# Kernel optimization log

Measured on AMD Instinct MI355X. Metric: run time of the kernel, lower is better.

## Reference

```python
import jax, jax.numpy as jnp
import numpy as np

B, T, N_DYN, D_H, D_Z, HID = 256, 1024, 20, 64, 128, 64


def setup_inputs() -> dict:
    key = jax.random.key(0)
    ks = jax.random.split(key, 12)

    def uinit(k, shape):
        lim = 1.0 / np.sqrt(shape[0])
        return jax.random.uniform(k, shape, jnp.float32, -lim, lim)

    return dict(
        z0=jax.random.normal(ks[0], (B, D_Z), jnp.float32),
        # non-decreasing event times per sample (hours)
        t_dyn=jnp.cumsum(jax.random.uniform(ks[1], (B, T), jnp.float32), axis=1),
        Y_dyn=jax.random.normal(ks[2], (B, T, N_DYN), jnp.float32),
        M_dyn=jax.random.uniform(ks[3], (B, T, N_DYN), jnp.float32),
        H_dyn=jax.random.normal(ks[4], (B, T, D_H), jnp.float32),  # h_path.query(t_k) per step
        dyn_lens=jax.random.randint(ks[5], (B,), 0, T),
        ode_W0=uinit(ks[6], (D_Z, HID)), ode_b0=jnp.zeros((HID,), jnp.float32),
        ode_W1=uinit(ks[7], (HID, HID)), ode_b1=jnp.zeros((HID,), jnp.float32),
        ode_W2=uinit(ks[8], (HID, D_Z)), ode_b2=jnp.zeros((D_Z,), jnp.float32),
        W_ih=uinit(ks[9], (2 * N_DYN + D_H, 3 * D_Z)), b_ih=jnp.zeros((3 * D_Z,), jnp.float32),
        W_hh=uinit(ks[10], (D_Z, 3 * D_Z)), b_hh=jnp.zeros((3 * D_Z,), jnp.float32),
    )


def reference(z0, t_dyn, Y_dyn, M_dyn, H_dyn, dyn_lens,
              ode_W0, ode_b0, ode_W1, ode_b1, ode_W2, ode_b2,
              W_ih, b_ih, W_hh, b_hh):
    def ode_f(z):
        h = jnp.tanh(z @ ode_W0 + ode_b0)
        h = jnp.tanh(h @ ode_W1 + ode_b1)
        return h @ ode_W2 + ode_b2

    def evolve(z, dt):  # dt: (B,1); single-step RK4 of dz/ds = f(z)*dt over s in [0,1]
        f = lambda z_: ode_f(z_) * dt
        k1 = f(z)
        k2 = f(z + 0.5 * k1)
        k3 = f(z + 0.5 * k2)
        k4 = f(z + k3)
        return z + (k1 + 2.0 * k2 + 2.0 * k3 + k4) / 6.0

    def gru(x, h):  # torch GRUCell math
        gi = x @ W_ih + b_ih
        gh = h @ W_hh + b_hh
        i_r, i_u, i_n = jnp.split(gi, 3, axis=-1)
        h_r, h_u, h_n = jnp.split(gh, 3, axis=-1)
        r = jax.nn.sigmoid(i_r + h_r)
        u = jax.nn.sigmoid(i_u + h_u)
        n = jnp.tanh(i_n + r * h_n)
        return (1.0 - u) * n + u * h

    def step(carry, xs):
        z, t_prev = carry
        t_k, y_k, m_k, h_k, k = xs
        dt = jnp.clip(t_k - t_prev, 0.0)[:, None]
        # at k==0 dt is exactly 0 so evolve(z,0)==z, matching the torch k==0 branch
        z_ode = evolve(z, dt)
        inp = jnp.concatenate([y_k, m_k, h_k], axis=-1)  # (B, 2*n_dyn + d_h)
        z_new = gru(inp, z_ode)
        active = (k < dyn_lens).astype(z.dtype)[:, None]
        z = z_new * active + z_ode * (1.0 - active)
        return (z, t_k), z

    Tm = t_dyn.shape[1]
    xs = (t_dyn.T,
          jnp.transpose(Y_dyn, (1, 0, 2)),
          jnp.transpose(M_dyn, (1, 0, 2)),
          jnp.transpose(H_dyn, (1, 0, 2)),
          jnp.arange(Tm))
    (z_final, _), Z = jax.lax.scan(step, (z0, t_dyn[:, 0]), xs)
    return z_final, jnp.transpose(Z, (1, 0, 2))  # (B,d_z), (B,T,d_z)
```

## Files before the change

kernel.cpp:

```cpp
#include <hip/hip_runtime.h>
#include <cstdint>
#include <cstddef>

#define B_    256
#define T_    1024
#define NDYN  20
#define DH    64
#define DZ    128
#define HIDN  64
#define GCOLS 384
#define XDIM  104
#define THR   512

#define WHH_LDS_G 17
#define WHH_REGA  32
#define WHH_REGB  28

__device__ __forceinline__ int cpad(int k) { return (k >> 4) * 20 + (k & 15); }

#define BAR() do { asm volatile("s_waitcnt lgkmcnt(0)" ::: "memory"); \
                   __builtin_amdgcn_s_barrier(); } while (0)

template<int CTRL, int XORMASK>
__device__ __forceinline__ float dpp_sum(float v) {
#if __has_builtin(__builtin_amdgcn_mov_dpp)
  int o = __builtin_amdgcn_mov_dpp(__float_as_int(v), CTRL, 0xF, 0xF, true);
  return v + __int_as_float(o);
#else
  return v + __shfl_xor(v, XORMASK);
#endif
}

__device__ __forceinline__ float tanh_fast(float x) {
  float a = __expf(-2.f * fabsf(x));
  return copysignf((1.f - a) / (1.f + a), x);
}
__device__ __forceinline__ float sigm(float x) { return 1.f / (1.f + __expf(-x)); }

__global__ __launch_bounds__(THR, 1) void odernn_kernel(
    const float* __restrict__ z0, const float* __restrict__ tdyn,
    const float* __restrict__ Y, const float* __restrict__ Mm,
    const float* __restrict__ Hh, const int* __restrict__ lens,
    const float* __restrict__ W0, const float* __restrict__ b0,
    const float* __restrict__ W1, const float* __restrict__ b1,
    const float* __restrict__ W2, const float* __restrict__ b2,
    const float* __restrict__ Wih, const float* __restrict__ bih,
    const float* __restrict__ Whh, const float* __restrict__ bhh,
    const float* __restrict__ gi_pre, float* __restrict__ out, int use_gi)
{
  const int tid = threadIdx.x;
  const int b   = blockIdx.x;

  __shared__ __align__(16) float vinP[160];
  __shared__ __align__(16) float h1P[80];
  __shared__ __align__(16) float h2P[80];
  __shared__ __align__(16) float zodeL[128];
  __shared__ float zcurL[128];
  __shared__ float gateL[384];
  __shared__ float gateN[128];
  __shared__ float xsL[112];
  __shared__ float dtL[T_];
  __shared__ __align__(16) float4 WhhP4[WHH_LDS_G * 384];

  const int jg0 = tid >> 3, p0 = tid & 7;
  const int j2  = tid >> 2, p2 = tid & 3;
  const int gcol = (tid < GCOLS) ? tid : 0;

  float w0r[16], w1r[8], w2r[16], whhA[WHH_REGA], whhB[WHH_REGB];

  if (tid < GCOLS) {
    #pragma unroll 1
    for (int g = 0; g < WHH_LDS_G; ++g) {
      float4 w;
      w.x = Whh[(4 * g + 0) * GCOLS + tid];
      w.y = Whh[(4 * g + 1) * GCOLS + tid];
      w.z = Whh[(4 * g + 2) * GCOLS + tid];
      w.w = Whh[(4 * g + 3) * GCOLS + tid];
      WhhP4[g * 384 + tid] = w;
    }
  }
  #pragma unroll
  for (int i = 0; i < WHH_REGA; ++i)
    whhA[i] = Whh[(4 * WHH_LDS_G + i) * GCOLS + gcol];
  #pragma unroll
  for (int i = 0; i < WHH_REGB; ++i)
    whhB[i] = Whh[(4 * WHH_LDS_G + WHH_REGA + i) * GCOLS + gcol];

  #pragma unroll
  for (int i = 0; i < 16; ++i) w0r[i] = W0[(16 * p0 + i) * HIDN + jg0];
  #pragma unroll
  for (int i = 0; i < 8; ++i)  w1r[i] = W1[(8 * p0 + i) * HIDN + jg0];
  #pragma unroll
  for (int i = 0; i < 16; ++i) w2r[i] = W2[(16 * p2 + i) * DZ + j2];

  const float* tdb = tdyn + (size_t)b * T_;
  for (int k = tid; k < T_; k += THR) {
    float tk = tdb[k];
    float tp = (k == 0) ? tk : tdb[k - 1];
    dtL[k] = fmaxf(tk - tp, 0.f);
  }

  float b0r = 0.f, b1r = 0.f, b2r = 0.f;
  if (p0 == 0) { b0r = b0[jg0]; b1r = b1[jg0]; }
  if (p2 == 0) b2r = b2[j2];
  const float bhhr = bhh[gcol];
  const float bihr = bih[gcol];
  const int   lenb = lens[b];

  if (tid < 128) {
    float zv = z0[(size_t)b * DZ + tid];
    vinP[cpad(tid)] = zv;
    zcurL[tid] = zv;
  }
  __syncthreads();

  float* Zbase = out + (size_t)B_ * DZ;

  #pragma unroll 1
  for (int t = 0; t < T_; ++t) {
    const size_t bt = (size_t)b * T_ + t;
    const float dt = dtL[t];

    float gival = 0.f;
    if (use_gi) {
      if (tid < GCOLS) gival = gi_pre[bt * GCOLS + tid];
    } else if (tid < XDIM) {
      float v;
      if (tid < 20)      v = Y[bt * NDYN + tid];
      else if (tid < 40) v = Mm[bt * NDYN + (tid - 20)];
      else               v = Hh[bt * DH + (tid - 40)];
      xsL[tid] = v;
    }

    float zreg = 0.f, kacc = 0.f;
    if (p2 == 0) zreg = zcurL[j2];

    #pragma unroll 1
    for (int e = 0; e < 4; ++e) {
      {
        const float4* vp = (const float4*)&vinP[p0 * 20];
        float a0 = 0.f;
        #pragma unroll
        for (int q = 0; q < 4; ++q) {
          float4 v = vp[q];
          a0 += w0r[4*q+0]*v.x + w0r[4*q+1]*v.y + w0r[4*q+2]*v.z + w0r[4*q+3]*v.w;
        }
        a0 = dpp_sum<0xB1,1>(a0); a0 = dpp_sum<0x4E,2>(a0); a0 = dpp_sum<0x141,4>(a0);
        if (p0 == 0)
          h1P[cpad(jg0)] = tanh_fast(a0 + b0r);
      }
      BAR();
      {
        const float4* hp = (const float4*)&h1P[cpad(8 * p0)];
        float4 v0 = hp[0], v1 = hp[1];
        float a0 = w1r[0]*v0.x + w1r[1]*v0.y + w1r[2]*v0.z + w1r[3]*v0.w
                 + w1r[4]*v1.x + w1r[5]*v1.y + w1r[6]*v1.z + w1r[7]*v1.w;
        a0 = dpp_sum<0xB1,1>(a0); a0 = dpp_sum<0x4E,2>(a0); a0 = dpp_sum<0x141,4>(a0);
        if (p0 == 0)
          h2P[cpad(jg0)] = tanh_fast(a0 + b1r);
      }
      BAR();
      {
        const float4* hp = (const float4*)&h2P[p2 * 20];
        float a0 = 0.f;
        #pragma unroll
        for (int q = 0; q < 4; ++q) {
          float4 v = hp[q];
          a0 += w2r[4*q+0]*v.x + w2r[4*q+1]*v.y + w2r[4*q+2]*v.z + w2r[4*q+3]*v.w;
        }
        a0 = dpp_sum<0xB1,1>(a0); a0 = dpp_sum<0x4E,2>(a0);
        if (p2 == 0) {
          const float kv = dt * (a0 + b2r);
          if (e == 0)      kacc = kv;
          else if (e == 3) kacc += kv;
          else             kacc += 2.f * kv;
          if (e < 3) {
            const float a = (e == 2) ? 1.f : 0.5f;
            vinP[cpad(j2)] = zreg + a * kv;
          } else {
            zodeL[j2] = zreg + kacc * (1.f / 6.f);
          }
        }
      }
      BAR();
    }

    if (tid < GCOLS) {
      float gh0 = bhhr, gh1 = 0.f;
      const float4* zq = (const float4*)zodeL;
      #pragma unroll 1
      for (int g = 0; g < WHH_LDS_G - 1; g += 2) {
        float4 w0 = WhhP4[g * 384 + tid];
        float4 w1 = WhhP4[(g + 1) * 384 + tid];
        float4 za = zq[g];
        float4 zb = zq[g + 1];
        gh0 += w0.x*za.x + w0.y*za.y + w0.z*za.z + w0.w*za.w;
        gh1 += w1.x*zb.x + w1.y*zb.y + w1.z*zb.z + w1.w*zb.w;
      }
      {
        float4 w0 = WhhP4[(WHH_LDS_G - 1) * 384 + tid];
        float4 za = zq[WHH_LDS_G - 1];
        gh0 += w0.x*za.x + w0.y*za.y + w0.z*za.z + w0.w*za.w;
      }
      #pragma unroll
      for (int q = 0; q < 8; ++q) {
        float4 z = zq[WHH_LDS_G + q];
        gh1 += whhA[4*q+0]*z.x + whhA[4*q+1]*z.y + whhA[4*q+2]*z.z + whhA[4*q+3]*z.w;
      }
      #pragma unroll
      for (int q = 0; q < 7; ++q) {
        float4 z = zq[WHH_LDS_G + 8 + q];
        gh0 += whhB[4*q+0]*z.x + whhB[4*q+1]*z.y + whhB[4*q+2]*z.z + whhB[4*q+3]*z.w;
      }
      float gh = gh0 + gh1;
      float gi;
      if (use_gi) gi = gival;
      else {
        gi = bihr;
        for (int i = 0; i < XDIM; ++i) gi += xsL[i] * Wih[(size_t)i * GCOLS + tid];
      }
      if (tid < 256) gateL[tid] = gi + gh;
      else { gateL[tid] = gh; gateN[tid - 256] = gi; }
    }
    BAR();

    if (tid < 128) {
      const float r  = sigm(gateL[tid]);
      const float uu = sigm(gateL[128 + tid]);
      const float n  = tanh_fast(gateN[tid] + r * gateL[256 + tid]);
      const float zo = zodeL[tid];
      const float zn = (1.f - uu) * n + uu * zo;
      const float znew = (t < lenb) ? zn : zo;
      vinP[cpad(tid)] = znew;
      zcurL[tid] = znew;
      Zbase[bt * DZ + tid] = znew;
    }
    BAR();
  }

  __syncthreads();
  if (tid < 128) out[(size_t)b * DZ + tid] = zcurL[tid];
}

__global__ __launch_bounds__(384) void gi_precompute(
    const float* __restrict__ Y, const float* __restrict__ Mm,
    const float* __restrict__ Hh, const float* __restrict__ Wih,
    const float* __restrict__ bih, float* __restrict__ gi)
{
  __shared__ float Xs[XDIM][16];
  const int tid = threadIdx.x;
  const size_t bt0 = (size_t)blockIdx.x * 16;
  for (int idx = tid; idx < XDIM * 16; idx += 384) {
    int r = idx & 15, c = idx >> 4;
    size_t bt = bt0 + r;
    float v;
    if (c < 20)      v = Y[bt * NDYN + c];
    else if (c < 40) v = Mm[bt * NDYN + (c - 20)];
    else             v = Hh[bt * DH + (c - 40)];
    Xs[c][r] = v;
  }
  __syncthreads();
  float acc[16];
  const float bv = bih[tid];
  #pragma unroll
  for (int r = 0; r < 16; ++r) acc[r] = bv;
  for (int i = 0; i < XDIM; ++i) {
    float w = Wih[i * GCOLS + tid];
    const float4* xp = (const float4*)(&Xs[i][0]);
    #pragma unroll
    for (int q = 0; q < 4; ++q) {
      float4 xv = xp[q];
      acc[4*q + 0] += xv.x * w;
      acc[4*q + 1] += xv.y * w;
      acc[4*q + 2] += xv.z * w;
      acc[4*q + 3] += xv.w * w;
    }
  }
  #pragma unroll
  for (int r = 0; r < 16; ++r) gi[(bt0 + r) * GCOLS + tid] = acc[r];
}

extern "C" void kernel_launch(void* const* d_in, const int* in_sizes, int n_in,
                              void* d_out, int out_size, void* d_ws, size_t ws_size,
                              hipStream_t stream) {
  const float* z0   = (const float*)d_in[0];
  const float* tdyn = (const float*)d_in[1];
  const float* Y    = (const float*)d_in[2];
  const float* Mm   = (const float*)d_in[3];
  const float* Hh   = (const float*)d_in[4];
  const int*   lens = (const int*)d_in[5];
  const float* W0   = (const float*)d_in[6];
  const float* b0   = (const float*)d_in[7];
  const float* W1   = (const float*)d_in[8];
  const float* b1   = (const float*)d_in[9];
  const float* W2   = (const float*)d_in[10];
  const float* b2   = (const float*)d_in[11];
  const float* Wih  = (const float*)d_in[12];
  const float* bih  = (const float*)d_in[13];
  const float* Whh  = (const float*)d_in[14];
  const float* bhh  = (const float*)d_in[15];
  float* out = (float*)d_out;

  const size_t gi_bytes = (size_t)B_ * T_ * GCOLS * sizeof(float);
  const int use_gi = (ws_size >= gi_bytes) ? 1 : 0;
  float* gi = (float*)d_ws;

  if (use_gi)
    gi_precompute<<<(B_ * T_) / 16, 384, 0, stream>>>(Y, Mm, Hh, Wih, bih, gi);

  odernn_kernel<<<B_, THR, 0, stream>>>(
      z0, tdyn, Y, Mm, Hh, lens, W0, b0, W1, b1, W2, b2,
      Wih, bih, Whh, bhh, use_gi ? gi : nullptr, out, use_gi);
}
```

Baseline: 4.727 ms.

## Remap GRU gate columns so gates combine via DPP, removing a barrier

Each group of four lanes now owns the r, u and n gate columns for one hidden unit, with Whh stored in LDS under an interleaved physical column index. Gate values are exchanged between lanes with DPP quad broadcasts instead of going through shared gate arrays, which removes one block barrier and an LDS round trip per timestep. All 512 threads now take part in the recurrent matvec, with lane 3 duplicating lane 2's work. The dot products are also split into more independent accumulators to shorten dependency chains.

Measured after the change: 4.929 ms. 4.3% more time.

```diff
diff --git a/kernel.cpp b/kernel.cpp
--- a/kernel.cpp
+++ b/kernel.cpp
@@ -28,6 +28,14 @@
   return v + __int_as_float(o);
 #else
   return v + __shfl_xor(v, XORMASK);
+#endif
+}
+template<int CTRL, int SRCLANE>
+__device__ __forceinline__ float dpp_mov(float v) {
+#if __has_builtin(__builtin_amdgcn_mov_dpp)
+  return __int_as_float(__builtin_amdgcn_mov_dpp(__float_as_int(v), CTRL, 0xF, 0xF, true));
+#else
+  return __shfl(v, (threadIdx.x & ~3) + SRCLANE, 64);
 #endif
 }
 
@@ -56,27 +64,27 @@
   __shared__ __align__(16) float h2P[80];
   __shared__ __align__(16) float zodeL[128];
   __shared__ float zcurL[128];
-  __shared__ float gateL[384];
-  __shared__ float gateN[128];
   __shared__ float xsL[112];
   __shared__ float dtL[T_];
   __shared__ __align__(16) float4 WhhP4[WHH_LDS_G * 384];
 
   const int jg0 = tid >> 3, p0 = tid & 7;
   const int j2  = tid >> 2, p2 = tid & 3;
-  const int gcol = (tid < GCOLS) ? tid : 0;
+  const int cg  = (p2 < 3) ? p2 : 2;
+  const int gcol = cg * 128 + j2;
+  const int physc = 3 * j2 + cg;
 
   float w0r[16], w1r[8], w2r[16], whhA[WHH_REGA], whhB[WHH_REGB];
 
-  if (tid < GCOLS) {
+  if (p2 < 3) {
     #pragma unroll 1
     for (int g = 0; g < WHH_LDS_G; ++g) {
       float4 w;
-      w.x = Whh[(4 * g + 0) * GCOLS + tid];
-      w.y = Whh[(4 * g + 1) * GCOLS + tid];
-      w.z = Whh[(4 * g + 2) * GCOLS + tid];
-      w.w = Whh[(4 * g + 3) * GCOLS + tid];
-      WhhP4[g * 384 + tid] = w;
+      w.x = Whh[(4 * g + 0) * GCOLS + gcol];
+      w.y = Whh[(4 * g + 1) * GCOLS + gcol];
+      w.z = Whh[(4 * g + 2) * GCOLS + gcol];
+      w.w = Whh[(4 * g + 3) * GCOLS + gcol];
+      WhhP4[g * 384 + physc] = w;
     }
   }
   #pragma unroll
@@ -123,7 +131,7 @@
 
     float gival = 0.f;
     if (use_gi) {
-      if (tid < GCOLS) gival = gi_pre[bt * GCOLS + tid];
+      gival = gi_pre[bt * GCOLS + gcol];
     } else if (tid < XDIM) {
       float v;
       if (tid < 20)      v = Y[bt * NDYN + tid];
@@ -132,19 +140,25 @@
       xsL[tid] = v;
     }
 
-    float zreg = 0.f, kacc = 0.f;
+    float zreg = 0.f, kacc = 0.f, zode_reg = 0.f;
     if (p2 == 0) zreg = zcurL[j2];
 
     #pragma unroll 1
     for (int e = 0; e < 4; ++e) {
       {
         const float4* vp = (const float4*)&vinP[p0 * 20];
-        float a0 = 0.f;
-        #pragma unroll
-        for (int q = 0; q < 4; ++q) {
-          float4 v = vp[q];
-          a0 += w0r[4*q+0]*v.x + w0r[4*q+1]*v.y + w0r[4*q+2]*v.z + w0r[4*q+3]*v.w;
-        }
+        float a00 = 0.f, a01 = 0.f;
+        {
+          float4 v0 = vp[0], v1 = vp[1];
+          a00 += w0r[0]*v0.x + w0r[1]*v0.y + w0r[2]*v0.z + w0r[3]*v0.w;
+          a01 += w0r[4]*v1.x + w0r[5]*v1.y + w0r[6]*v1.z + w0r[7]*v1.w;
+        }
+        {
+          float4 v2 = vp[2], v3 = vp[3];
+          a00 += w0r[8]*v2.x + w0r[9]*v2.y + w0r[10]*v2.z + w0r[11]*v2.w;
+          a01 += w0r[12]*v3.x + w0r[13]*v3.y + w0r[14]*v3.z + w0r[15]*v3.w;
+        }
+        float a0 = a00 + a01;
         a0 = dpp_sum<0xB1,1>(a0); a0 = dpp_sum<0x4E,2>(a0); a0 = dpp_sum<0x141,4>(a0);
         if (p0 == 0)
           h1P[cpad(jg0)] = tanh_fast(a0 + b0r);
@@ -153,8 +167,9 @@
       {
         const float4* hp = (const float4*)&h1P[cpad(8 * p0)];
         float4 v0 = hp[0], v1 = hp[1];
-        float a0 = w1r[0]*v0.x + w1r[1]*v0.y + w1r[2]*v0.z + w1r[3]*v0.w
-                 + w1r[4]*v1.x + w1r[5]*v1.y + w1r[6]*v1.z + w1r[7]*v1.w;
+        float a00 = w1r[0]*v0.x + w1r[1]*v0.y + w1r[2]*v0.z + w1r[3]*v0.w;
+        float a01 = w1r[4]*v1.x + w1r[5]*v1.y + w1r[6]*v1.z + w1r[7]*v1.w;
+        float a0 = a00 + a01;
         a0 = dpp_sum<0xB1,1>(a0); a0 = dpp_sum<0x4E,2>(a0); a0 = dpp_sum<0x141,4>(a0);
         if (p0 == 0)
           h2P[cpad(jg0)] = tanh_fast(a0 + b1r);
@@ -162,12 +177,18 @@
       BAR();
       {
         const float4* hp = (const float4*)&h2P[p2 * 20];
-        float a0 = 0.f;
-        #pragma unroll
-        for (int q = 0; q < 4; ++q) {
-          float4 v = hp[q];
-          a0 += w2r[4*q+0]*v.x + w2r[4*q+1]*v.y + w2r[4*q+2]*v.z + w2r[4*q+3]*v.w;
-        }
+        float a00 = 0.f, a01 = 0.f;
+        {
+          float4 v0 = hp[0], v1 = hp[1];
+          a00 += w2r[0]*v0.x + w2r[1]*v0.y + w2r[2]*v0.z + w2r[3]*v0.w;
+          a01 += w2r[4]*v1.x + w2r[5]*v1.y + w2r[6]*v1.z + w2r[7]*v1.w;
+        }
+        {
+          float4 v2 = hp[2], v3 = hp[3];
+          a00 += w2r[8]*v2.x + w2r[9]*v2.y + w2r[10]*v2.z + w2r[11]*v2.w;
+          a01 += w2r[12]*v3.x + w2r[13]*v3.y + w2r[14]*v3.z + w2r[15]*v3.w;
+        }
+        float a0 = a00 + a01;
         a0 = dpp_sum<0xB1,1>(a0); a0 = dpp_sum<0x4E,2>(a0);
         if (p2 == 0) {
           const float kv = dt * (a0 + b2r);
@@ -178,62 +199,64 @@
             const float a = (e == 2) ? 1.f : 0.5f;
             vinP[cpad(j2)] = zreg + a * kv;
           } else {
-            zodeL[j2] = zreg + kacc * (1.f / 6.f);
+            zode_reg = zreg + kacc * (1.f / 6.f);
+            zodeL[j2] = zode_reg;
           }
         }
       }
       BAR();
     }
 
-    if (tid < GCOLS) {
-      float gh0 = bhhr, gh1 = 0.f;
+    {
+      float gh0 = bhhr, gh1 = 0.f, gh2 = 0.f, gh3 = 0.f;
       const float4* zq = (const float4*)zodeL;
       #pragma unroll 1
       for (int g = 0; g < WHH_LDS_G - 1; g += 2) {
-        float4 w0 = WhhP4[g * 384 + tid];
-        float4 w1 = WhhP4[(g + 1) * 384 + tid];
+        float4 w0 = WhhP4[g * 384 + physc];
+        float4 w1 = WhhP4[(g + 1) * 384 + physc];
         float4 za = zq[g];
         float4 zb = zq[g + 1];
         gh0 += w0.x*za.x + w0.y*za.y + w0.z*za.z + w0.w*za.w;
         gh1 += w1.x*zb.x + w1.y*zb.y + w1.z*zb.z + w1.w*zb.w;
       }
       {
-        float4 w0 = WhhP4[(WHH_LDS_G - 1) * 384 + tid];
+        float4 w0 = WhhP4[(WHH_LDS_G - 1) * 384 + physc];
         float4 za = zq[WHH_LDS_G - 1];
         gh0 += w0.x*za.x + w0.y*za.y + w0.z*za.z + w0.w*za.w;
       }
       #pragma unroll
       for (int q = 0; q < 8; ++q) {
         float4 z = zq[WHH_LDS_G + q];
-        gh1 += whhA[4*q+0]*z.x + whhA[4*q+1]*z.y + whhA[4*q+2]*z.z + whhA[4*q+3]*z.w;
+        gh2 += whhA[4*q+0]*z.x + whhA[4*q+1]*z.y + whhA[4*q+2]*z.z + whhA[4*q+3]*z.w;
       }
       #pragma unroll
       for (int q = 0; q < 7; ++q) {
         float4 z = zq[WHH_LDS_G + 8 + q];
-        gh0 += whhB[4*q+0]*z.x + whhB[4*q+1]*z.y + whhB[4*q+2]*z.z + whhB[4*q+3]*z.w;
-      }
-      float gh = gh0 + gh1;
+        gh3 += whhB[4*q+0]*z.x + whhB[4*q+1]*z.y + whhB[4*q+2]*z.z + whhB[4*q+3]*z.w;
+      }
+      float gh = (gh0 + gh1) + (gh2 + gh3);
       float gi;
       if (use_gi) gi = gival;
       else {
         gi = bihr;
-        for (int i = 0; i < XDIM; ++i) gi += xsL[i] * Wih[(size_t)i * GCOLS + tid];
-      }
-      if (tid < 256) gateL[tid] = gi + gh;
-      else { gateL[tid] = gh; gateN[tid - 256] = gi; }
-    }
-    BAR();
-
-    if (tid < 128) {
-      const float r  = sigm(gateL[tid]);
-      const float uu = sigm(gateL[128 + tid]);
-      const float n  = tanh_fast(gateN[tid] + r * gateL[256 + tid]);
-      const float zo = zodeL[tid];
-      const float zn = (1.f - uu) * n + uu * zo;
-      const float znew = (t < lenb) ? zn : zo;
-      vinP[cpad(tid)] = znew;
-      zcurL[tid] = znew;
-      Zbase[bt * DZ + tid] = znew;
+        for (int i = 0; i < XDIM; ++i) gi += xsL[i] * Wih[(size_t)i * GCOLS + gcol];
+      }
+      const float smain = (cg == 2) ? gh : (gh + gi);
+      const float saux  = gi;
+      const float u_s = dpp_mov<0x55, 1>(smain);
+      const float ghn = dpp_mov<0xAA, 2>(smain);
+      const float gin = dpp_mov<0xAA, 2>(saux);
+      if (p2 == 0) {
+        const float r  = sigm(smain);
+        const float uu = sigm(u_s);
+        const float n  = tanh_fast(gin + r * ghn);
+        const float zo = zode_reg;
+        const float zn = (1.f - uu) * n + uu * zo;
+        const float znew = (t < lenb) ? zn : zo;
+        vinP[cpad(j2)] = znew;
+        zcurL[j2] = znew;
+        Zbase[bt * DZ + j2] = znew;
+      }
     }
     BAR();
   }
```
